# Kernel optimization log

Measured on AMD Instinct MI355X. Metric: run time of the kernel, lower is better.

## Reference

```python
import jax, jax.numpy as jnp
import numpy as np

N_NODES = 50000
N_EDGES = 800000
N_HEADS = 8
MULT = 16  # multiplicity per degree
F_KEY_NFEAT = MULT * 1 + MULT * 3  # 64


def setup_inputs() -> dict:
    key = jax.random.key(0)
    ks = jax.random.split(key, 7)
    return {
        "v0": jax.random.normal(ks[0], (N_EDGES, MULT, 1), dtype=jnp.float32),
        "v1": jax.random.normal(ks[1], (N_EDGES, MULT, 3), dtype=jnp.float32),
        "k0": jax.random.normal(ks[2], (N_EDGES, MULT, 1), dtype=jnp.float32),
        "k1": jax.random.normal(ks[3], (N_EDGES, MULT, 3), dtype=jnp.float32),
        "q0": jax.random.normal(ks[4], (N_NODES, MULT, 1), dtype=jnp.float32),
        "q1": jax.random.normal(ks[5], (N_NODES, MULT, 3), dtype=jnp.float32),
        "edge_index": jax.random.randint(ks[6], (2, N_EDGES), 0, N_NODES, dtype=jnp.int32),
    }


def _fiber2head(d0, d1, n_heads):
    # [X, m, 2d+1] -> [X, H, (m/H)*(2d+1)], concat over degrees on last axis
    x0 = d0.reshape(d0.shape[0], n_heads, -1)
    x1 = d1.reshape(d1.shape[0], n_heads, -1)
    return jnp.concatenate([x0, x1], axis=-1)


def reference(v0, v1, k0, k1, q0, q1, edge_index):
    row, col = edge_index[0], edge_index[1]
    N = q0.shape[0]
    H = N_HEADS

    k = _fiber2head(k0, k1, H)          # [E, H, 8]
    q = _fiber2head(q0, q1, H)          # [N, H, 8]

    # per-edge attention logits (dot over channel dim), scaled by sqrt(f_key.n_features)
    e = (k * q[col]).sum(axis=2) / np.float32(np.sqrt(F_KEY_NFEAT))  # [E, H]
    e = jnp.exp(e)
    s = jax.ops.segment_sum(e, row, num_segments=N)  # [N, H]
    a = e / s[row]                                   # [E, H]
    attn = a[:, :, None, None]                       # [E, H, 1, 1]

    mH = MULT // H
    # degree-0 messages: [E, H, m/H, 1]
    out0 = jax.ops.segment_sum(attn * v0.reshape(-1, H, mH, 1), col, num_segments=N)
    out0 = out0.reshape(N, MULT, 1)
    # degree-1 messages: [E, H, m/H, 3]
    out1 = jax.ops.segment_sum(attn * v1.reshape(-1, H, mH, 3), col, num_segments=N)
    out1 = out1.reshape(N, MULT, 3)
    return out0, out1
```

## Files before the change

### kernel.cpp

```cpp
#include <hip/hip_runtime.h>
#include <hip/hip_fp16.h>

#define N_NODES 50000
#define N_EDGES 800000

struct alignas(16) H8 { __half h[8]; };

__global__ __launch_bounds__(256) void k_hist(const int* __restrict__ ei,
                                              int* __restrict__ cnt_r,
                                              int* __restrict__ cnt_c)
{
    int e = blockIdx.x * blockDim.x + threadIdx.x;
    if (e >= N_EDGES) return;
    atomicAdd(cnt_r + ei[e], 1);
    atomicAdd(cnt_c + ei[N_EDGES + e], 1);
}

#define SCAN_T 1024
#define SCAN_I 8
__global__ __launch_bounds__(SCAN_T) void k_scan2(int* cnt_r, int* off_r,
                                                  int* cnt_c, int* off_c)
{
    int* cnt = blockIdx.x ? cnt_c : cnt_r;
    int* off = blockIdx.x ? off_c : off_r;
    __shared__ int wsum[16];
    __shared__ int carry_s;
    const int n = N_NODES;
    int wid = threadIdx.x >> 6, lane = threadIdx.x & 63;
    if (threadIdx.x == 0) carry_s = 0;
    __syncthreads();
    for (int base = 0; base < n; base += SCAN_T * SCAN_I) {
        int idx0 = base + threadIdx.x * SCAN_I;
        int v[SCAN_I];
        int sum = 0;
        #pragma unroll
        for (int j = 0; j < SCAN_I; ++j) {
            int i = idx0 + j;
            v[j] = (i < n) ? cnt[i] : 0;
            sum += v[j];
        }
        int x = sum;
        #pragma unroll
        for (int d = 1; d < 64; d <<= 1) {
            int t = __shfl_up(x, d);
            if (lane >= d) x += t;
        }
        if (lane == 63) wsum[wid] = x;
        __syncthreads();
        if (wid == 0 && lane < 16) {
            int y = wsum[lane];
            #pragma unroll
            for (int d = 1; d < 16; d <<= 1) {
                int t = __shfl_up(y, d);
                if (lane >= d) y += t;
            }
            wsum[lane] = y;
        }
        __syncthreads();
        int wave_excl = wid ? wsum[wid - 1] : 0;
        int run = carry_s + wave_excl + (x - sum);
        #pragma unroll
        for (int j = 0; j < SCAN_I; ++j) {
            int i = idx0 + j;
            if (i < n) { off[i] = run; cnt[i] = run; }
            run += v[j];
        }
        __syncthreads();
        if (threadIdx.x == 0) carry_s += wsum[15];
        __syncthreads();
    }
    if (threadIdx.x == 0) off[n] = carry_s;
}

__global__ __launch_bounds__(256) void k_logits_fill(
    const float* __restrict__ k0, const float* __restrict__ k1,
    const float* __restrict__ q0, const float* __restrict__ q1,
    const int* __restrict__ ei,
    int* __restrict__ cur_r, int* __restrict__ cur_c,
    int* __restrict__ xlink_r, int2* __restrict__ eid_c2,
    H8* __restrict__ e_c)
{
    int e = blockIdx.x * blockDim.x + threadIdx.x;
    if (e >= N_EDGES) return;
    int row = ei[e];
    int col = ei[N_EDGES + e];

    int pr = atomicAdd(cur_r + row, 1);
    int pc = atomicAdd(cur_c + col, 1);

    const float4* k0v = (const float4*)(k0 + (size_t)e   * 16);
    const float4* q0v = (const float4*)(q0 + (size_t)col * 16);
    const float4* k1v = (const float4*)(k1 + (size_t)e   * 48);
    const float4* q1v = (const float4*)(q1 + (size_t)col * 48);

    float acc[8];
    #pragma unroll
    for (int h = 0; h < 8; ++h) acc[h] = 0.f;

    #pragma unroll
    for (int i = 0; i < 4; ++i) {
        float4 kv = k0v[i];
        float4 qv = q0v[i];
        acc[(4*i+0)/2] += kv.x * qv.x;
        acc[(4*i+1)/2] += kv.y * qv.y;
        acc[(4*i+2)/2] += kv.z * qv.z;
        acc[(4*i+3)/2] += kv.w * qv.w;
    }
    #pragma unroll
    for (int j = 0; j < 12; ++j) {
        float4 kv = k1v[j];
        float4 qv = q1v[j];
        acc[(4*j+0)/6] += kv.x * qv.x;
        acc[(4*j+1)/6] += kv.y * qv.y;
        acc[(4*j+2)/6] += kv.z * qv.z;
        acc[(4*j+3)/6] += kv.w * qv.w;
    }

    H8 pack;
    #pragma unroll
    for (int h = 0; h < 8; ++h) pack.h[h] = __float2half(__expf(acc[h] * 0.125f));

    e_c[pc] = pack;
    int2 pr2; pr2.x = e; pr2.y = row;
    eid_c2[pc] = pr2;
    xlink_r[pr] = pc;
}

__global__ __launch_bounds__(256) void k_s(const __half* __restrict__ e_half,
                                           const int* __restrict__ off_r,
                                           const int* __restrict__ xlink_r,
                                           float* __restrict__ rs)
{
    int t = blockIdx.x * blockDim.x + threadIdx.x;
    int node = t >> 3;
    int h = t & 7;
    if (node >= N_NODES) return;
    int beg = off_r[node], end = off_r[node + 1];
    float acc = 0.f;
    int i = beg;
    for (; i + 8 <= end; i += 8) {
        float x0 = __half2float(e_half[(size_t)xlink_r[i + 0] * 8 + h]);
        float x1 = __half2float(e_half[(size_t)xlink_r[i + 1] * 8 + h]);
        float x2 = __half2float(e_half[(size_t)xlink_r[i + 2] * 8 + h]);
        float x3 = __half2float(e_half[(size_t)xlink_r[i + 3] * 8 + h]);
        float x4 = __half2float(e_half[(size_t)xlink_r[i + 4] * 8 + h]);
        float x5 = __half2float(e_half[(size_t)xlink_r[i + 5] * 8 + h]);
        float x6 = __half2float(e_half[(size_t)xlink_r[i + 6] * 8 + h]);
        float x7 = __half2float(e_half[(size_t)xlink_r[i + 7] * 8 + h]);
        acc += ((x0 + x1) + (x2 + x3)) + ((x4 + x5) + (x6 + x7));
    }
    for (; i < end; ++i) {
        acc += __half2float(e_half[(size_t)xlink_r[i] * 8 + h]);
    }
    rs[(size_t)node * 8 + h] = 1.0f / acc;
}

__global__ __launch_bounds__(256) void k_out(
    const float* __restrict__ v0, const float* __restrict__ v1,
    const __half* __restrict__ e_half, const float* __restrict__ rs,
    const int* __restrict__ off_c, const int2* __restrict__ eid_c2,
    float* __restrict__ out0, float* __restrict__ out1)
{
    int wave = (blockIdx.x * blockDim.x + threadIdx.x) >> 6;
    int lane = threadIdx.x & 63;
    if (wave >= N_NODES) return;
    bool is0 = lane < 16;
    int f1 = lane - 16;
    int head = is0 ? (lane >> 1) : (f1 / 6);
    const float* __restrict__ vbase = is0 ? (v0 + lane) : (v1 + f1);
    int vstride = is0 ? 16 : 48;

    int beg = off_c[wave], end = off_c[wave + 1];
    float acc = 0.f;
    int i = beg;
    for (; i + 8 <= end; i += 8) {
        int2 p0 = eid_c2[i + 0];
        int2 p1 = eid_c2[i + 1];
        int2 p2 = eid_c2[i + 2];
        int2 p3 = eid_c2[i + 3];
        int2 p4 = eid_c2[i + 4];
        int2 p5 = eid_c2[i + 5];
        int2 p6 = eid_c2[i + 6];
        int2 p7 = eid_c2[i + 7];
        float ev0 = __half2float(e_half[(size_t)(i + 0) * 8 + head]);
        float ev1 = __half2float(e_half[(size_t)(i + 1) * 8 + head]);
        float ev2 = __half2float(e_half[(size_t)(i + 2) * 8 + head]);
        float ev3 = __half2float(e_half[(size_t)(i + 3) * 8 + head]);
        float ev4 = __half2float(e_half[(size_t)(i + 4) * 8 + head]);
        float ev5 = __half2float(e_half[(size_t)(i + 5) * 8 + head]);
        float ev6 = __half2float(e_half[(size_t)(i + 6) * 8 + head]);
        float ev7 = __half2float(e_half[(size_t)(i + 7) * 8 + head]);
        float w0 = __builtin_nontemporal_load(vbase + (size_t)p0.x * vstride);
        float w1 = __builtin_nontemporal_load(vbase + (size_t)p1.x * vstride);
        float w2 = __builtin_nontemporal_load(vbase + (size_t)p2.x * vstride);
        float w3 = __builtin_nontemporal_load(vbase + (size_t)p3.x * vstride);
        float w4 = __builtin_nontemporal_load(vbase + (size_t)p4.x * vstride);
        float w5 = __builtin_nontemporal_load(vbase + (size_t)p5.x * vstride);
        float w6 = __builtin_nontemporal_load(vbase + (size_t)p6.x * vstride);
        float w7 = __builtin_nontemporal_load(vbase + (size_t)p7.x * vstride);
        float a0 = ev0 * rs[(size_t)p0.y * 8 + head];
        float a1 = ev1 * rs[(size_t)p1.y * 8 + head];
        float a2 = ev2 * rs[(size_t)p2.y * 8 + head];
        float a3 = ev3 * rs[(size_t)p3.y * 8 + head];
        float a4 = ev4 * rs[(size_t)p4.y * 8 + head];
        float a5 = ev5 * rs[(size_t)p5.y * 8 + head];
        float a6 = ev6 * rs[(size_t)p6.y * 8 + head];
        float a7 = ev7 * rs[(size_t)p7.y * 8 + head];
        acc += a0 * w0; acc += a1 * w1; acc += a2 * w2; acc += a3 * w3;
        acc += a4 * w4; acc += a5 * w5; acc += a6 * w6; acc += a7 * w7;
    }
    for (; i + 4 <= end; i += 4) {
        int2 p0 = eid_c2[i + 0];
        int2 p1 = eid_c2[i + 1];
        int2 p2 = eid_c2[i + 2];
        int2 p3 = eid_c2[i + 3];
        float ev0 = __half2float(e_half[(size_t)(i + 0) * 8 + head]);
        float ev1 = __half2float(e_half[(size_t)(i + 1) * 8 + head]);
        float ev2 = __half2float(e_half[(size_t)(i + 2) * 8 + head]);
        float ev3 = __half2float(e_half[(size_t)(i + 3) * 8 + head]);
        float w0 = __builtin_nontemporal_load(vbase + (size_t)p0.x * vstride);
        float w1 = __builtin_nontemporal_load(vbase + (size_t)p1.x * vstride);
        float w2 = __builtin_nontemporal_load(vbase + (size_t)p2.x * vstride);
        float w3 = __builtin_nontemporal_load(vbase + (size_t)p3.x * vstride);
        float a0 = ev0 * rs[(size_t)p0.y * 8 + head];
        float a1 = ev1 * rs[(size_t)p1.y * 8 + head];
        float a2 = ev2 * rs[(size_t)p2.y * 8 + head];
        float a3 = ev3 * rs[(size_t)p3.y * 8 + head];
        acc += a0 * w0; acc += a1 * w1; acc += a2 * w2; acc += a3 * w3;
    }
    for (; i < end; ++i) {
        int2 p0 = eid_c2[i];
        acc += __half2float(e_half[(size_t)i * 8 + head])
             * rs[(size_t)p0.y * 8 + head]
             * __builtin_nontemporal_load(vbase + (size_t)p0.x * vstride);
    }
    if (is0) out0[(size_t)wave * 16 + lane] = acc;
    else     out1[(size_t)wave * 48 + f1]   = acc;
}

extern "C" void kernel_launch(void* const* d_in, const int* in_sizes, int n_in,
                              void* d_out, int out_size, void* d_ws, size_t ws_size,
                              hipStream_t stream) {
    const float* v0 = (const float*)d_in[0];
    const float* v1 = (const float*)d_in[1];
    const float* k0 = (const float*)d_in[2];
    const float* k1 = (const float*)d_in[3];
    const float* q0 = (const float*)d_in[4];
    const float* q1 = (const float*)d_in[5];
    const int*   ei = (const int*)d_in[6];

    float* out0 = (float*)d_out;
    float* out1 = out0 + (size_t)N_NODES * 16;

    char* ws = (char*)d_ws;
    int*    cnt_r   = (int*)   (ws + 0);
    int*    cnt_c   = (int*)   (ws + 200000);
    int*    off_r   = (int*)   (ws + 400000);
    int*    off_c   = (int*)   (ws + 600016);
    int*    xlink_r = (int*)   (ws + 800032);
    int2*   eid_c2  = (int2*)  (ws + 4000032);
    H8*     e_c     = (H8*)    (ws + 10400032);
    float*  rs      = (float*) (ws + 23200032);

    hipMemsetAsync(cnt_r, 0, 400000, stream);

    const int block = 256;
    const int gridE = (N_EDGES + block - 1) / block;

    k_hist<<<gridE, block, 0, stream>>>(ei, cnt_r, cnt_c);
    k_scan2<<<2, SCAN_T, 0, stream>>>(cnt_r, off_r, cnt_c, off_c);
    k_logits_fill<<<gridE, block, 0, stream>>>(k0, k1, q0, q1, ei,
                                               cnt_r, cnt_c, xlink_r, eid_c2, e_c);
    k_s<<<(N_NODES * 8 + block - 1) / block, block, 0, stream>>>(
        (const __half*)e_c, off_r, xlink_r, rs);
    k_out<<<(N_NODES * 64 + block - 1) / block, block, 0, stream>>>(
        v0, v1, (const __half*)e_c, rs, off_c, eid_c2, out0, out1);
}
```

Baseline: 698.7 us.

## Split fill from logits and compute logits in col-sorted order

Splits the fused fill-and-logits kernel in two. The first kernel does the atomic slot assignment and writes a packed record (edge id, plus row and col in 16 bits each). The second kernel walks the edges in col-sorted order, so consecutive threads mostly read the same q rows and get better cache locality, while e_c writes become contiguous. This costs an extra kernel launch and a pass over the record array, k0/k1 reads become scattered, and the 16-bit packing of node ids is only correct while node counts stay below 65536.

```diff
diff --git a/kernel.cpp b/kernel.cpp
--- a/kernel.cpp
+++ b/kernel.cpp
@@ -72,21 +72,33 @@
     if (threadIdx.x == 0) off[n] = carry_s;
 }
 
-__global__ __launch_bounds__(256) void k_logits_fill(
-    const float* __restrict__ k0, const float* __restrict__ k1,
-    const float* __restrict__ q0, const float* __restrict__ q1,
-    const int* __restrict__ ei,
-    int* __restrict__ cur_r, int* __restrict__ cur_c,
-    int* __restrict__ xlink_r, int2* __restrict__ eid_c2,
-    H8* __restrict__ e_c)
+__global__ __launch_bounds__(256) void k_fill(const int* __restrict__ ei,
+                                              int* __restrict__ cur_r,
+                                              int* __restrict__ cur_c,
+                                              int2* __restrict__ pc8,
+                                              int* __restrict__ xlink_r)
 {
     int e = blockIdx.x * blockDim.x + threadIdx.x;
     if (e >= N_EDGES) return;
     int row = ei[e];
     int col = ei[N_EDGES + e];
-
     int pr = atomicAdd(cur_r + row, 1);
     int pc = atomicAdd(cur_c + col, 1);
+    int2 rec; rec.x = e; rec.y = row | (col << 16);
+    pc8[pc] = rec;
+    xlink_r[pr] = pc;
+}
+
+__global__ __launch_bounds__(256) void k_logits(
+    const float* __restrict__ k0, const float* __restrict__ k1,
+    const float* __restrict__ q0, const float* __restrict__ q1,
+    const int2* __restrict__ pc8, H8* __restrict__ e_c)
+{
+    int pc = blockIdx.x * blockDim.x + threadIdx.x;
+    if (pc >= N_EDGES) return;
+    int2 rec = pc8[pc];
+    int e   = rec.x;
+    int col = ((unsigned)rec.y) >> 16;
 
     const float4* k0v = (const float4*)(k0 + (size_t)e   * 16);
     const float4* q0v = (const float4*)(q0 + (size_t)col * 16);
@@ -119,11 +131,7 @@
     H8 pack;
     #pragma unroll
     for (int h = 0; h < 8; ++h) pack.h[h] = __float2half(__expf(acc[h] * 0.125f));
-
     e_c[pc] = pack;
-    int2 pr2; pr2.x = e; pr2.y = row;
-    eid_c2[pc] = pr2;
-    xlink_r[pr] = pc;
 }
 
 __global__ __launch_bounds__(256) void k_s(const __half* __restrict__ e_half,
@@ -158,7 +166,7 @@
 __global__ __launch_bounds__(256) void k_out(
     const float* __restrict__ v0, const float* __restrict__ v1,
     const __half* __restrict__ e_half, const float* __restrict__ rs,
-    const int* __restrict__ off_c, const int2* __restrict__ eid_c2,
+    const int* __restrict__ off_c, const int2* __restrict__ pc8,
     float* __restrict__ out0, float* __restrict__ out1)
 {
     int wave = (blockIdx.x * blockDim.x + threadIdx.x) >> 6;
@@ -174,14 +182,14 @@
     float acc = 0.f;
     int i = beg;
     for (; i + 8 <= end; i += 8) {
-        int2 p0 = eid_c2[i + 0];
-        int2 p1 = eid_c2[i + 1];
-        int2 p2 = eid_c2[i + 2];
-        int2 p3 = eid_c2[i + 3];
-        int2 p4 = eid_c2[i + 4];
-        int2 p5 = eid_c2[i + 5];
-        int2 p6 = eid_c2[i + 6];
-        int2 p7 = eid_c2[i + 7];
+        int2 p0 = pc8[i + 0];
+        int2 p1 = pc8[i + 1];
+        int2 p2 = pc8[i + 2];
+        int2 p3 = pc8[i + 3];
+        int2 p4 = pc8[i + 4];
+        int2 p5 = pc8[i + 5];
+        int2 p6 = pc8[i + 6];
+        int2 p7 = pc8[i + 7];
         float ev0 = __half2float(e_half[(size_t)(i + 0) * 8 + head]);
         float ev1 = __half2float(e_half[(size_t)(i + 1) * 8 + head]);
         float ev2 = __half2float(e_half[(size_t)(i + 2) * 8 + head]);
@@ -198,22 +206,22 @@
         float w5 = __builtin_nontemporal_load(vbase + (size_t)p5.x * vstride);
         float w6 = __builtin_nontemporal_load(vbase + (size_t)p6.x * vstride);
         float w7 = __builtin_nontemporal_load(vbase + (size_t)p7.x * vstride);
-        float a0 = ev0 * rs[(size_t)p0.y * 8 + head];
-        float a1 = ev1 * rs[(size_t)p1.y * 8 + head];
-        float a2 = ev2 * rs[(size_t)p2.y * 8 + head];
-        float a3 = ev3 * rs[(size_t)p3.y * 8 + head];
-        float a4 = ev4 * rs[(size_t)p4.y * 8 + head];
-        float a5 = ev5 * rs[(size_t)p5.y * 8 + head];
-        float a6 = ev6 * rs[(size_t)p6.y * 8 + head];
-        float a7 = ev7 * rs[(size_t)p7.y * 8 + head];
+        float a0 = ev0 * rs[(size_t)(p0.y & 0xFFFF) * 8 + head];
+        float a1 = ev1 * rs[(size_t)(p1.y & 0xFFFF) * 8 + head];
+        float a2 = ev2 * rs[(size_t)(p2.y & 0xFFFF) * 8 + head];
+        float a3 = ev3 * rs[(size_t)(p3.y & 0xFFFF) * 8 + head];
+        float a4 = ev4 * rs[(size_t)(p4.y & 0xFFFF) * 8 + head];
+        float a5 = ev5 * rs[(size_t)(p5.y & 0xFFFF) * 8 + head];
+        float a6 = ev6 * rs[(size_t)(p6.y & 0xFFFF) * 8 + head];
+        float a7 = ev7 * rs[(size_t)(p7.y & 0xFFFF) * 8 + head];
         acc += a0 * w0; acc += a1 * w1; acc += a2 * w2; acc += a3 * w3;
         acc += a4 * w4; acc += a5 * w5; acc += a6 * w6; acc += a7 * w7;
     }
     for (; i + 4 <= end; i += 4) {
-        int2 p0 = eid_c2[i + 0];
-        int2 p1 = eid_c2[i + 1];
-        int2 p2 = eid_c2[i + 2];
-        int2 p3 = eid_c2[i + 3];
+        int2 p0 = pc8[i + 0];
+        int2 p1 = pc8[i + 1];
+        int2 p2 = pc8[i + 2];
+        int2 p3 = pc8[i + 3];
         float ev0 = __half2float(e_half[(size_t)(i + 0) * 8 + head]);
         float ev1 = __half2float(e_half[(size_t)(i + 1) * 8 + head]);
         float ev2 = __half2float(e_half[(size_t)(i + 2) * 8 + head]);
@@ -222,16 +230,16 @@
         float w1 = __builtin_nontemporal_load(vbase + (size_t)p1.x * vstride);
         float w2 = __builtin_nontemporal_load(vbase + (size_t)p2.x * vstride);
         float w3 = __builtin_nontemporal_load(vbase + (size_t)p3.x * vstride);
-        float a0 = ev0 * rs[(size_t)p0.y * 8 + head];
-        float a1 = ev1 * rs[(size_t)p1.y * 8 + head];
-        float a2 = ev2 * rs[(size_t)p2.y * 8 + head];
-        float a3 = ev3 * rs[(size_t)p3.y * 8 + head];
+        float a0 = ev0 * rs[(size_t)(p0.y & 0xFFFF) * 8 + head];
+        float a1 = ev1 * rs[(size_t)(p1.y & 0xFFFF) * 8 + head];
+        float a2 = ev2 * rs[(size_t)(p2.y & 0xFFFF) * 8 + head];
+        float a3 = ev3 * rs[(size_t)(p3.y & 0xFFFF) * 8 + head];
         acc += a0 * w0; acc += a1 * w1; acc += a2 * w2; acc += a3 * w3;
     }
     for (; i < end; ++i) {
-        int2 p0 = eid_c2[i];
+        int2 p0 = pc8[i];
         acc += __half2float(e_half[(size_t)i * 8 + head])
-             * rs[(size_t)p0.y * 8 + head]
+             * rs[(size_t)(p0.y & 0xFFFF) * 8 + head]
              * __builtin_nontemporal_load(vbase + (size_t)p0.x * vstride);
     }
     if (is0) out0[(size_t)wave * 16 + lane] = acc;
@@ -258,7 +266,7 @@
     int*    off_r   = (int*)   (ws + 400000);
     int*    off_c   = (int*)   (ws + 600016);
     int*    xlink_r = (int*)   (ws + 800032);
-    int2*   eid_c2  = (int2*)  (ws + 4000032);
+    int2*   pc8     = (int2*)  (ws + 4000032);
     H8*     e_c     = (H8*)    (ws + 10400032);
     float*  rs      = (float*) (ws + 23200032);
 
@@ -269,10 +277,10 @@
 
     k_hist<<<gridE, block, 0, stream>>>(ei, cnt_r, cnt_c);
     k_scan2<<<2, SCAN_T, 0, stream>>>(cnt_r, off_r, cnt_c, off_c);
-    k_logits_fill<<<gridE, block, 0, stream>>>(k0, k1, q0, q1, ei,
-                                               cnt_r, cnt_c, xlink_r, eid_c2, e_c);
+    k_fill<<<gridE, block, 0, stream>>>(ei, cnt_r, cnt_c, pc8, xlink_r);
+    k_logits<<<gridE, block, 0, stream>>>(k0, k1, q0, q1, pc8, e_c);
     k_s<<<(N_NODES * 8 + block - 1) / block, block, 0, stream>>>(
         (const __half*)e_c, off_r, xlink_r, rs);
     k_out<<<(N_NODES * 64 + block - 1) / block, block, 0, stream>>>(
-        v0, v1, (const __half*)e_c, rs, off_c, eid_c2, out0, out1);
-}
+        v0, v1, (const __half*)e_c, rs, off_c, pc8, out0, out1);
+}
```

New measurement: 704.9 us. About the same (+0.9%).
